# Performance work log

Measured on AMD Instinct MI355X. Metric: run time of the kernel, lower is better.

## Reference

```python
import jax, jax.numpy as jnp
import numpy as np

SIGMA = 0.01        # config['fscore_sigma']
FSCORE_W = 0.1      # config['fscore_weight']
TASK_W = 1.0        # config['task_weight']
DOMAIN_W = 0.1      # config['domain_weight']


def setup_inputs() -> dict:
    key = jax.random.key(0)
    ks = jax.random.split(key, 11)
    B, N, M, F = 8, 4096, 4096, 512
    H1, H2, D = 256, 128, 6
    return {
        "pred_pc": jax.random.normal(ks[0], (B, N, 3), jnp.float32),
        "target_pc": jax.random.normal(ks[1], (B, M, 3), jnp.float32),
        "domain_features": jax.random.normal(ks[2], (B, F), jnp.float32),
        "dataset_weights": jax.random.uniform(ks[3], (B,), jnp.float32, 0.9, 1.2),
        "W1": jax.random.normal(ks[4], (F, H1), jnp.float32) * 0.02,
        "b1": jnp.zeros((H1,), jnp.float32),
        "W2": jax.random.normal(ks[5], (H1, H2), jnp.float32) * 0.02,
        "b2": jnp.zeros((H2,), jnp.float32),
        "W3": jax.random.normal(ks[6], (H2, D), jnp.float32) * 0.02,
        "b3": jnp.zeros((D,), jnp.float32),
        "domain_labels": jax.random.randint(ks[7], (B,), 0, D),
    }


def _chamfer_mins(pred, tgt):
    # pred: [B,N,3], tgt: [B,M,3] -> squared pairwise dists [B,N,M], then dual mins
    d = (jnp.sum(pred ** 2, axis=2)[:, :, None]
         + jnp.sum(tgt ** 2, axis=2)[:, None, :]
         - 2.0 * jnp.einsum('bnd,bmd->bnm', pred, tgt))
    return jnp.min(d, axis=2), jnp.min(d, axis=1)   # [B,N], [B,M]


def reference(pred_pc, target_pc, domain_features, dataset_weights,
              W1, b1, W2, b2, W3, b3, domain_labels):
    min_a, min_b = _chamfer_mins(pred_pc, target_pc)
    c = 2.0 * SIGMA * SIGMA
    soft_a = jnp.exp(-min_a / c)
    soft_b = jnp.exp(-min_b / c)

    # batch-level task loss (compute_reconstruction_loss on full batch)
    chamfer = jnp.mean(min_a) + jnp.mean(min_b)
    prec = jnp.mean(soft_a)
    rec = jnp.mean(soft_b)
    fscore = 2.0 * prec * rec / (prec + rec + 1e-8)
    task = chamfer + FSCORE_W * (1.0 - fscore)

    # per-sample dataset-weighted loss (vectorized form of the Python loop)
    ch_i = jnp.mean(min_a, axis=1) + jnp.mean(min_b, axis=1)
    p_i = jnp.mean(soft_a, axis=1)
    r_i = jnp.mean(soft_b, axis=1)
    f_i = 2.0 * p_i * r_i / (p_i + r_i + 1e-8)
    loss_i = ch_i + FSCORE_W * (1.0 - f_i)
    dataset_weighted = jnp.mean(dataset_weights * loss_i)

    # domain loss: GRL is identity in forward; classifier in eval mode (dropout off)
    h = jax.nn.relu(domain_features @ W1 + b1)
    h = jax.nn.relu(h @ W2 + b2)
    logits = h @ W3 + b3
    logp = jax.nn.log_softmax(logits, axis=-1)
    domain = -jnp.mean(jnp.take_along_axis(logp, domain_labels[:, None], axis=1))

    total = TASK_W * task + DOMAIN_W * domain + dataset_weighted
    return total
```

## Files before the change

kernel.cpp:

```cpp
#include <hip/hip_runtime.h>
#include <math.h>

#define B 8
#define NPTS 4096
#define QPT 4
#define QC  4
#define THREADS 256

typedef float v2f __attribute__((ext_vector_type(2)));
typedef float v4f __attribute__((ext_vector_type(4)));

__device__ __forceinline__ float min3f(float a, float b, float c) {
  return fminf(fminf(a, b), c);
}

#if __has_builtin(__builtin_elementwise_fma)
__device__ __forceinline__ v2f fma2(v2f a, v2f b, v2f c) {
  return __builtin_elementwise_fma(a, b, c);
}
#else
__device__ __forceinline__ v2f fma2(v2f a, v2f b, v2f c) {
  v2f r; r.x = __builtin_fmaf(a.x, b.x, c.x); r.y = __builtin_fmaf(a.y, b.y, c.y);
  return r;
}
#endif

#define VLO(v) __builtin_shufflevector(v, v, 0, 1)
#define VHI(v) __builtin_shufflevector(v, v, 2, 3)


template<int S, int LOG2S>
__global__ __launch_bounds__(THREADS, 4) void k1_kernel(
    const float* __restrict__ pred, const float* __restrict__ targ,
    const float* __restrict__ x, const float* __restrict__ W1,
    float* __restrict__ partial, float* __restrict__ sums64,
    float* __restrict__ h1p) {
  constexpr int REFS = NPTS / S;
  const int tid = threadIdx.x;
  const int bid = blockIdx.x;

  __shared__ __align__(16) float sx[REFS];
  __shared__ __align__(16) float sy[REFS];
  __shared__ __align__(16) float sz[REFS];
  __shared__ __align__(16) float sw[REFS];
  __shared__ float xs[64];

  if (bid < 64) {
    if (bid == 0 && tid < 64) sums64[tid] = 0.f;
    int b = bid >> 3, kc = bid & 7;
    if (tid < 64) xs[tid] = x[b * 512 + kc * 64 + tid];
    __syncthreads();
    float acc = 0.f;
    const float* w = W1 + (size_t)(kc * 64) * 256 + tid;
#pragma unroll 8
    for (int k = 0; k < 64; ++k) acc = fmaf(xs[k], w[k * 256], acc);
    h1p[(b * 8 + kc) * 256 + tid] = acc;
    __syncthreads();
  }

  int xcd  = bid & 7;
  int spl  = (bid >> 3) & (S - 1);
  int cs   = bid >> (3 + LOG2S);
  int gid  = cs * 8 + xcd;
  int qc   = gid & (QC - 1);
  int b    = (gid >> 2) & 7;
  int dir  = gid >> 5;
  const float* qp = dir ? targ : pred;
  const float* rp = dir ? pred : targ;

  const float* qb = qp + (size_t)b * NPTS * 3;
  int q0 = qc * (QPT * THREADS) + tid;
  float qx[QPT], qy[QPT], qz[QPT];
#pragma unroll
  for (int i = 0; i < QPT; ++i) {
    int q = q0 + i * THREADS;
    qx[i] = qb[q * 3 + 0];
    qy[i] = qb[q * 3 + 1];
    qz[i] = qb[q * 3 + 2];
  }

  const float* rb = rp + ((size_t)b * NPTS + (size_t)spl * REFS) * 3;
  for (int i = tid; i < REFS; i += THREADS) {
    float xx = rb[i * 3 + 0], yy = rb[i * 3 + 1], zz = rb[i * 3 + 2];
    sx[i] = xx; sy[i] = yy; sz[i] = zz;
    sw[i] = 0.5f * (xx * xx + yy * yy + zz * zz);
  }

  float qn[QPT], vmin[QPT];
  v2f bx[QPT], by[QPT], bz[QPT];
#pragma unroll
  for (int i = 0; i < QPT; ++i) {
    qn[i] = fmaf(qx[i], qx[i], fmaf(qy[i], qy[i], qz[i] * qz[i]));
    bx[i] = (v2f){-qx[i], -qx[i]};
    by[i] = (v2f){-qy[i], -qy[i]};
    bz[i] = (v2f){-qz[i], -qz[i]};
    vmin[i] = 3.4e38f;
  }
  __syncthreads();

  for (int j = 0; j < REFS; j += 8) {
    v4f xA = *(const v4f*)(sx + j), xB = *(const v4f*)(sx + j + 4);
    v4f yA = *(const v4f*)(sy + j), yB = *(const v4f*)(sy + j + 4);
    v4f zA = *(const v4f*)(sz + j), zB = *(const v4f*)(sz + j + 4);
    v4f wA = *(const v4f*)(sw + j), wB = *(const v4f*)(sw + j + 4);
    v2f x01 = VLO(xA), x23 = VHI(xA), x45 = VLO(xB), x67 = VHI(xB);
    v2f y01 = VLO(yA), y23 = VHI(yA), y45 = VLO(yB), y67 = VHI(yB);
    v2f z01 = VLO(zA), z23 = VHI(zA), z45 = VLO(zB), z67 = VHI(zB);
    v2f w01 = VLO(wA), w23 = VHI(wA), w45 = VLO(wB), w67 = VHI(wB);
#pragma unroll
    for (int i = 0; i < QPT; ++i) {
      v2f s01 = fma2(bx[i], x01, fma2(by[i], y01, fma2(bz[i], z01, w01)));
      v2f s23 = fma2(bx[i], x23, fma2(by[i], y23, fma2(bz[i], z23, w23)));
      v2f s45 = fma2(bx[i], x45, fma2(by[i], y45, fma2(bz[i], z45, w45)));
      v2f s67 = fma2(bx[i], x67, fma2(by[i], y67, fma2(bz[i], z67, w67)));
      float m0 = min3f(s01.x, s01.y, s23.x);
      float m1 = min3f(s23.y, s45.x, s45.y);
      float m2 = min3f(s67.x, s67.y, m0);
      vmin[i] = min3f(m1, m2, vmin[i]);
    }
  }

  size_t base = (((size_t)dir * B + b) * S + spl) * NPTS;
#pragma unroll
  for (int i = 0; i < QPT; ++i)
    partial[base + q0 + i * THREADS] = fmaf(2.f, vmin[i], qn[i]);
}

template<int S>
__global__ __launch_bounds__(THREADS) void k2_kernel(
    const float* __restrict__ partial, float* __restrict__ sums64,
    const float* __restrict__ h1p, const float* __restrict__ b1,
    const float* __restrict__ W2, const float* __restrict__ b2,
    const float* __restrict__ W3, const float* __restrict__ b3,
    const int* __restrict__ labels, const float* __restrict__ wgt,
    float* __restrict__ out) {
  constexpr int NBLK = 272;
  const int id = blockIdx.x;
  const int tid = threadIdx.x;
  __shared__ float red[8];
  __shared__ float hs[128];
  __shared__ bool is_last;

  if (id >= 256) {
    int lid = id - 256;
    int b = lid >> 1, half = lid & 1;
    if (tid < 128) {
      int k = half * 128 + tid;
      float a = b1[k];
#pragma unroll
      for (int p = 0; p < 8; ++p) a += h1p[(b * 8 + p) * 256 + k];
      hs[tid] = fmaxf(a, 0.f);
    }
    __syncthreads();
    if (tid < 128) {
      float acc = 0.f;
      const float* w = W2 + (size_t)(half * 128) * 128 + tid;
#pragma unroll 8
      for (int k = 0; k < 128; ++k) acc = fmaf(hs[k], w[k * 128], acc);
      float* h2p = sums64 + 64 + 64 * 256;
      h2p[(b * 2 + half) * 128 + tid] = acc;
    }
  } else {
    int chunk = id & 15;
    int b   = (id >> 4) & 7;
    int dir = id >> 7;
    size_t pb = ((size_t)dir * B + b) * S * NPTS;
    int q = chunk * 256 + tid;

    float v[S];
#pragma unroll
    for (int s = 0; s < S; ++s)
      v[s] = partial[pb + (size_t)s * NPTS + q];
    float m = v[0];
#pragma unroll
    for (int s = 1; s < S; ++s) m = fminf(m, v[s]);
    float s_min = m;
    float s_soft = __expf(-5000.0f * m);

    for (int off = 32; off > 0; off >>= 1) {
      s_min  += __shfl_down(s_min,  off);
      s_soft += __shfl_down(s_soft, off);
    }
    int wave = tid >> 6, lane = tid & 63;
    if (lane == 0) { red[wave * 2] = s_min; red[wave * 2 + 1] = s_soft; }
    __syncthreads();
    if (tid == 0) {
      float a = 0.f, c = 0.f;
      for (int wv = 0; wv < 4; ++wv) { a += red[wv * 2]; c += red[wv * 2 + 1]; }
      atomicAdd(&sums64[(dir * B + b) * 2 + 0], a);
      atomicAdd(&sums64[(dir * B + b) * 2 + 1], c);
    }
  }

  __threadfence();
  __syncthreads();
  if (tid == 0) {
    unsigned t = atomicAdd((unsigned*)(sums64 + 32), 1u);
    is_last = (t == NBLK - 1);
  }
  __syncthreads();
  if (!is_last) return;
  __threadfence();

  __shared__ float h2s[8 * 128];
  __shared__ float lg[48];
  __shared__ float nlls[8];
  volatile const float* vh2 = (volatile const float*)(sums64 + 64 + 64 * 256);

  for (int i = tid; i < 1024; i += THREADS) {
    int bb = i >> 7, j = i & 127;
    float a = b2[j] + vh2[(bb * 2 + 0) * 128 + j] + vh2[(bb * 2 + 1) * 128 + j];
    h2s[i] = fmaxf(a, 0.f);
  }
  __syncthreads();
  if (tid < 48) {
    int bb = tid / 6, d = tid % 6;
    float acc = b3[d];
#pragma unroll 8
    for (int k = 0; k < 128; ++k)
      acc = fmaf(h2s[bb * 128 + k], W3[k * 6 + d], acc);
    lg[tid] = acc;
  }
  __syncthreads();
  if (tid < 8) {
    int bb = tid;
    float mx = lg[bb * 6];
    for (int d = 1; d < 6; ++d) mx = fmaxf(mx, lg[bb * 6 + d]);
    float se = 0.f;
    for (int d = 0; d < 6; ++d) se += __expf(lg[bb * 6 + d] - mx);
    int lab = labels[bb];
    nlls[bb] = -(lg[bb * 6 + lab] - mx - __logf(se));
  }
  __syncthreads();
  if (tid == 0) {
    volatile const float* vs = (volatile const float*)sums64;
    float chamfer = 0.f, prec = 0.f, rec = 0.f, dsw = 0.f, dom = 0.f;
    for (int bb = 0; bb < B; ++bb) {
      float sa  = vs[(0 * B + bb) * 2 + 0];
      float ssa = vs[(0 * B + bb) * 2 + 1];
      float sb  = vs[(1 * B + bb) * 2 + 0];
      float ssb = vs[(1 * B + bb) * 2 + 1];
      float ma = sa / 4096.f, mb = sb / 4096.f;
      float p = ssa / 4096.f, r = ssb / 4096.f;
      chamfer += ma + mb;
      prec += p; rec += r;
      float f_i = 2.f * p * r / (p + r + 1e-8f);
      float loss_i = ma + mb + 0.1f * (1.f - f_i);
      dsw += wgt[bb] * loss_i;
      dom += nlls[bb];
    }
    chamfer *= (1.f / B); prec *= (1.f / B); rec *= (1.f / B);
    dsw *= (1.f / B); dom *= (1.f / B);
    float fscore = 2.f * prec * rec / (prec + rec + 1e-8f);
    float task = chamfer + 0.1f * (1.f - fscore);
    out[0] = 1.0f * task + 0.1f * dom + dsw;
  }
}

template<int S, int LOG2S>
static void run_pipeline(const float* pred, const float* targ, const float* x,
                         const float* wgt, const float* W1, const float* b1,
                         const float* W2, const float* b2, const float* W3,
                         const float* b3, const int* labels, float* out,
                         char* ws, hipStream_t stream) {
  float* partial = (float*)ws;
  float* sums64  = partial + (size_t)2 * B * S * NPTS;
  float* h1p     = sums64 + 64;

  hipLaunchKernelGGL((k1_kernel<S, LOG2S>), dim3(64 * S), dim3(THREADS),
                     0, stream, pred, targ, x, W1, partial, sums64, h1p);
  hipLaunchKernelGGL((k2_kernel<S>), dim3(272), dim3(THREADS), 0, stream,
                     partial, sums64, h1p, b1, W2, b2, W3, b3, labels, wgt,
                     out);
}

extern "C" void kernel_launch(void* const* d_in, const int* in_sizes, int n_in,
                              void* d_out, int out_size, void* d_ws, size_t ws_size,
                              hipStream_t stream) {
  const float* pred   = (const float*)d_in[0];
  const float* targ   = (const float*)d_in[1];
  const float* x      = (const float*)d_in[2];
  const float* wgt    = (const float*)d_in[3];
  const float* W1     = (const float*)d_in[4];
  const float* b1     = (const float*)d_in[5];
  const float* W2     = (const float*)d_in[6];
  const float* b2     = (const float*)d_in[7];
  const float* W3     = (const float*)d_in[8];
  const float* b3     = (const float*)d_in[9];
  const int*   labels = (const int*)d_in[10];
  float* out = (float*)d_out;
  char* ws = (char*)d_ws;

  auto need = [](int S) {
    return ((size_t)2 * B * S * NPTS + 64 + 64 * 256 + 16 * 128) * sizeof(float);
  };
  if (ws_size >= need(32))
    run_pipeline<32, 5>(pred, targ, x, wgt, W1, b1, W2, b2, W3, b3, labels,
                        out, ws, stream);
  else if (ws_size >= need(16))
    run_pipeline<16, 4>(pred, targ, x, wgt, W1, b1, W2, b2, W3, b3, labels,
                        out, ws, stream);
  else
    run_pipeline<8, 3>(pred, targ, x, wgt, W1, b1, W2, b2, W3, b3, labels,
                       out, ws, stream);
}
```

Measured before the change: 133.4 us.

## Use AoS float4 refs, 8 queries per thread, separate MLP blocks, drop S=32

The chamfer kernel now stores reference points as interleaved float4 (x,y,z,half-norm) in LDS instead of four SoA arrays, and replaces packed v2f FMAs with scalar FMAs. Each thread handles 8 queries instead of 4, doubling register reuse of each LDS load. The first 64 blocks now only do the MLP layer and return, with the chamfer work moved to separate blocks, and the S=32 split option is removed so S defaults to 16. The trade-off is more registers per thread, fewer blocks, and losing packed-FMA throughput and the XCD-aware block mapping.

New measurement: 131.7 us. No clear change (-1.3%).

```diff
diff --git a/kernel.cpp b/kernel.cpp
--- a/kernel.cpp
+++ b/kernel.cpp
@@ -3,30 +3,13 @@
 
 #define B 8
 #define NPTS 4096
-#define QPT 4
-#define QC  4
+#define QPT 8
 #define THREADS 256
-
-typedef float v2f __attribute__((ext_vector_type(2)));
-typedef float v4f __attribute__((ext_vector_type(4)));
+#define NGRP 32
 
 __device__ __forceinline__ float min3f(float a, float b, float c) {
   return fminf(fminf(a, b), c);
 }
-
-#if __has_builtin(__builtin_elementwise_fma)
-__device__ __forceinline__ v2f fma2(v2f a, v2f b, v2f c) {
-  return __builtin_elementwise_fma(a, b, c);
-}
-#else
-__device__ __forceinline__ v2f fma2(v2f a, v2f b, v2f c) {
-  v2f r; r.x = __builtin_fmaf(a.x, b.x, c.x); r.y = __builtin_fmaf(a.y, b.y, c.y);
-  return r;
-}
-#endif
-
-#define VLO(v) __builtin_shufflevector(v, v, 0, 1)
-#define VHI(v) __builtin_shufflevector(v, v, 2, 3)
 
 
 template<int S, int LOG2S>
@@ -37,17 +20,14 @@
     float* __restrict__ h1p) {
   constexpr int REFS = NPTS / S;
   const int tid = threadIdx.x;
-  const int bid = blockIdx.x;
-
-  __shared__ __align__(16) float sx[REFS];
-  __shared__ __align__(16) float sy[REFS];
-  __shared__ __align__(16) float sz[REFS];
-  __shared__ __align__(16) float sw[REFS];
+  const int id = blockIdx.x;
+
+  __shared__ float4 refs[REFS];
   __shared__ float xs[64];
 
-  if (bid < 64) {
-    if (bid == 0 && tid < 64) sums64[tid] = 0.f;
-    int b = bid >> 3, kc = bid & 7;
+  if (id < 64) {
+    if (id == 0 && tid < 64) sums64[tid] = 0.f;
+    int b = id >> 3, kc = id & 7;
     if (tid < 64) xs[tid] = x[b * 512 + kc * 64 + tid];
     __syncthreads();
     float acc = 0.f;
@@ -55,75 +35,61 @@
 #pragma unroll 8
     for (int k = 0; k < 64; ++k) acc = fmaf(xs[k], w[k * 256], acc);
     h1p[(b * 8 + kc) * 256 + tid] = acc;
-    __syncthreads();
-  }
-
-  int xcd  = bid & 7;
-  int spl  = (bid >> 3) & (S - 1);
-  int cs   = bid >> (3 + LOG2S);
-  int gid  = cs * 8 + xcd;
-  int qc   = gid & (QC - 1);
-  int b    = (gid >> 2) & 7;
-  int dir  = gid >> 5;
+    return;
+  }
+
+  int cid = id - 64;
+  int spl = cid & (S - 1);
+  int g   = cid >> LOG2S;
+  int qc  = g & 1;
+  int b   = (g >> 1) & 7;
+  int dir = g >> 4;
   const float* qp = dir ? targ : pred;
   const float* rp = dir ? pred : targ;
 
+  const float* rb = rp + ((size_t)b * NPTS + (size_t)spl * REFS) * 3;
+  for (int i = tid; i < REFS; i += THREADS) {
+    float xx = rb[i * 3 + 0], yy = rb[i * 3 + 1], zz = rb[i * 3 + 2];
+    refs[i] = make_float4(xx, yy, zz, 0.5f * (xx * xx + yy * yy + zz * zz));
+  }
+  __syncthreads();
+
   const float* qb = qp + (size_t)b * NPTS * 3;
   int q0 = qc * (QPT * THREADS) + tid;
-  float qx[QPT], qy[QPT], qz[QPT];
+  float qx[QPT], qy[QPT], qz[QPT], vmin[QPT];
 #pragma unroll
   for (int i = 0; i < QPT; ++i) {
     int q = q0 + i * THREADS;
     qx[i] = qb[q * 3 + 0];
     qy[i] = qb[q * 3 + 1];
     qz[i] = qb[q * 3 + 2];
-  }
-
-  const float* rb = rp + ((size_t)b * NPTS + (size_t)spl * REFS) * 3;
-  for (int i = tid; i < REFS; i += THREADS) {
-    float xx = rb[i * 3 + 0], yy = rb[i * 3 + 1], zz = rb[i * 3 + 2];
-    sx[i] = xx; sy[i] = yy; sz[i] = zz;
-    sw[i] = 0.5f * (xx * xx + yy * yy + zz * zz);
-  }
-
-  float qn[QPT], vmin[QPT];
-  v2f bx[QPT], by[QPT], bz[QPT];
+    vmin[i] = 3.4e38f;
+  }
+
+  for (int jr = 0; jr < REFS; jr += 8) {
+    float4 t[8];
+#pragma unroll
+    for (int u = 0; u < 8; ++u) t[u] = refs[jr + u];
+#pragma unroll
+    for (int i = 0; i < QPT; ++i) {
+      float s[8];
+#pragma unroll
+      for (int u = 0; u < 8; ++u)
+        s[u] = fmaf(-qx[i], t[u].x,
+               fmaf(-qy[i], t[u].y, fmaf(-qz[i], t[u].z, t[u].w)));
+      float m0 = min3f(s[0], s[1], s[2]);
+      float m1 = min3f(s[3], s[4], s[5]);
+      float m2 = min3f(s[6], s[7], m0);
+      vmin[i] = min3f(m1, m2, vmin[i]);
+    }
+  }
+
+  size_t base = (((size_t)dir * B + b) * S + spl) * NPTS;
 #pragma unroll
   for (int i = 0; i < QPT; ++i) {
-    qn[i] = fmaf(qx[i], qx[i], fmaf(qy[i], qy[i], qz[i] * qz[i]));
-    bx[i] = (v2f){-qx[i], -qx[i]};
-    by[i] = (v2f){-qy[i], -qy[i]};
-    bz[i] = (v2f){-qz[i], -qz[i]};
-    vmin[i] = 3.4e38f;
-  }
-  __syncthreads();
-
-  for (int j = 0; j < REFS; j += 8) {
-    v4f xA = *(const v4f*)(sx + j), xB = *(const v4f*)(sx + j + 4);
-    v4f yA = *(const v4f*)(sy + j), yB = *(const v4f*)(sy + j + 4);
-    v4f zA = *(const v4f*)(sz + j), zB = *(const v4f*)(sz + j + 4);
-    v4f wA = *(const v4f*)(sw + j), wB = *(const v4f*)(sw + j + 4);
-    v2f x01 = VLO(xA), x23 = VHI(xA), x45 = VLO(xB), x67 = VHI(xB);
-    v2f y01 = VLO(yA), y23 = VHI(yA), y45 = VLO(yB), y67 = VHI(yB);
-    v2f z01 = VLO(zA), z23 = VHI(zA), z45 = VLO(zB), z67 = VHI(zB);
-    v2f w01 = VLO(wA), w23 = VHI(wA), w45 = VLO(wB), w67 = VHI(wB);
-#pragma unroll
-    for (int i = 0; i < QPT; ++i) {
-      v2f s01 = fma2(bx[i], x01, fma2(by[i], y01, fma2(bz[i], z01, w01)));
-      v2f s23 = fma2(bx[i], x23, fma2(by[i], y23, fma2(bz[i], z23, w23)));
-      v2f s45 = fma2(bx[i], x45, fma2(by[i], y45, fma2(bz[i], z45, w45)));
-      v2f s67 = fma2(bx[i], x67, fma2(by[i], y67, fma2(bz[i], z67, w67)));
-      float m0 = min3f(s01.x, s01.y, s23.x);
-      float m1 = min3f(s23.y, s45.x, s45.y);
-      float m2 = min3f(s67.x, s67.y, m0);
-      vmin[i] = min3f(m1, m2, vmin[i]);
-    }
-  }
-
-  size_t base = (((size_t)dir * B + b) * S + spl) * NPTS;
-#pragma unroll
-  for (int i = 0; i < QPT; ++i)
-    partial[base + q0 + i * THREADS] = fmaf(2.f, vmin[i], qn[i]);
+    float qn = fmaf(qx[i], qx[i], fmaf(qy[i], qy[i], qz[i] * qz[i]));
+    partial[base + q0 + i * THREADS] = fmaf(2.f, vmin[i], qn);
+  }
 }
 
 template<int S>
@@ -267,7 +233,7 @@
   float* sums64  = partial + (size_t)2 * B * S * NPTS;
   float* h1p     = sums64 + 64;
 
-  hipLaunchKernelGGL((k1_kernel<S, LOG2S>), dim3(64 * S), dim3(THREADS),
+  hipLaunchKernelGGL((k1_kernel<S, LOG2S>), dim3(64 + NGRP * S), dim3(THREADS),
                      0, stream, pred, targ, x, W1, partial, sums64, h1p);
   hipLaunchKernelGGL((k2_kernel<S>), dim3(272), dim3(THREADS), 0, stream,
                      partial, sums64, h1p, b1, W2, b2, W3, b3, labels, wgt,
@@ -294,10 +260,7 @@
   auto need = [](int S) {
     return ((size_t)2 * B * S * NPTS + 64 + 64 * 256 + 16 * 128) * sizeof(float);
   };
-  if (ws_size >= need(32))
-    run_pipeline<32, 5>(pred, targ, x, wgt, W1, b1, W2, b2, W3, b3, labels,
-                        out, ws, stream);
-  else if (ws_size >= need(16))
+  if (ws_size >= need(16))
     run_pipeline<16, 4>(pred, targ, x, wgt, W1, b1, W2, b2, W3, b3, labels,
                         out, ws, stream);
   else
```
